# Performance work log

Hardware: AMD Instinct MI355X
Metric: run time of the kernel (lower is better)

Reference implementation:

```python
import jax, jax.numpy as jnp
import numpy as np

B, C, H, W = 2, 128, 64, 64


def setup_inputs() -> dict:
    key = jax.random.key(0)
    ks = jax.random.split(key, 16)
    s = 1.0 / np.sqrt(C)
    d = {
        "x": jax.random.normal(ks[0], (B, C, H, W), jnp.float32),
        "y": jax.random.normal(ks[1], (B, C, H, W), jnp.float32),
    }
    names = ["qr", "qi", "kr", "ki", "vr", "vi"]
    for i, n in enumerate(names):
        d["W" + n] = jax.random.normal(ks[2 + 2 * i], (C, C), jnp.float32) * s
        d["b" + n] = jax.random.normal(ks[3 + 2 * i], (C,), jnp.float32) * s
    return d


def _lin(t, Wt, bt):
    # t: [b, n, c]; torch Linear: t @ W^T + b
    return jnp.einsum("bnc,dc->bnd", t, Wt) + bt


def reference(x, y, Wqr, bqr, Wqi, bqi, Wkr, bkr, Wki, bki, Wvr, bvr, Wvi, bvi):
    b, c, h, w = x.shape
    xf = jnp.fft.fft2(x)  # over last two axes (h, w)
    yf = jnp.fft.fft2(y)
    # b c h w -> b (h w) c
    def flat(t):
        return t.transpose(0, 2, 3, 1).reshape(b, h * w, c)
    xr, xi = flat(xf.real), flat(xf.imag)
    yr, yi = flat(yf.real), flat(yf.imag)

    Qr = _lin(xr, Wqr, bqr) - _lin(xi, Wqi, bqi)
    Qi = _lin(xi, Wqr, bqr) + _lin(xr, Wqi, bqi)
    Kr = _lin(yr, Wkr, bkr) - _lin(yi, Wki, bki)
    Ki = _lin(yi, Wkr, bkr) + _lin(yr, Wki, bki)
    Vr = _lin(yr, Wvr, bvr) - _lin(yi, Wvi, bvi)
    Vi = _lin(yi, Wvr, bvr) + _lin(yr, Wvi, bvi)

    sr = jnp.einsum("bnc,bmc->bnm", Qr, Kr) - jnp.einsum("bnc,bmc->bnm", Qi, Ki)
    si = jnp.einsum("bnc,bmc->bnm", Qr, Ki) + jnp.einsum("bnc,bmc->bnm", Qi, Kr)
    scores = jnp.sqrt(sr * sr + si * si + 1e-8)
    attn = jax.nn.softmax(scores, axis=-1)

    out_r = jnp.einsum("bnm,bmc->bnc", attn, Vr)
    out_i = jnp.einsum("bnm,bmc->bnc", attn, Vi)
    out_c = jax.lax.complex(out_r, out_i)
    # b (h w) c -> b c h w
    out_c = out_c.reshape(b, h, w, c).transpose(0, 3, 1, 2)
    return jnp.fft.ifft2(out_c).real
```

## Files before the change

kernel.cpp:

```cpp
#include <hip/hip_runtime.h>
#include <math.h>


#define PI2 6.283185307179586f

typedef __attribute__((ext_vector_type(8))) short short8;
typedef __attribute__((ext_vector_type(4))) float f32x4;

#define MFMA16(A,B,C) __builtin_amdgcn_mfma_f32_16x16x32_bf16((A),(B),(C),0,0,0)

__device__ inline unsigned short f2bf(float x){
  union{float f; unsigned int u;} a; a.f = x;
  unsigned int r = (a.u + 0x7fffu + ((a.u>>16)&1u)) >> 16;
  return (unsigned short)r;
}
__device__ inline float bf2f(unsigned short h){
  union{unsigned int u; float f;} a; a.u = ((unsigned int)h)<<16; return a.f;
}
__device__ inline short8 neg8(short8 x){
  union{short8 v; unsigned int u[4];} a; a.v = x;
  a.u[0]^=0x80008000u; a.u[1]^=0x80008000u; a.u[2]^=0x80008000u; a.u[3]^=0x80008000u;
  return a.v;
}
__device__ inline void gload_lds16(const void* g, void* lds){
  __builtin_amdgcn_global_load_lds((const __attribute__((address_space(1))) unsigned int*)g,
                                   (__attribute__((address_space(3))) unsigned int*)lds,
                                   16, 0, 0);
}

__global__ __launch_bounds__(256) void dft2_fwd_kernel(
    const float* __restrict__ x, const float* __restrict__ y,
    float* __restrict__ xr, float* __restrict__ xi,
    float* __restrict__ yr, float* __restrict__ yi)
{
  __shared__ float Xs[4096];
  __shared__ float Tr[4096], Ti[4096];
  __shared__ float twc[64], tws[64];
  int blk = blockIdx.x;
  const float* src; float *outr, *outi;
  int plane;
  if (blk < 256) { src = x; outr = xr; outi = xi; plane = blk; }
  else           { src = y; outr = yr; outi = yi; plane = blk - 256; }
  int b = plane >> 7, c = plane & 127;
  int t = threadIdx.x;
  if (t < 64) {
    float ang = -PI2 * (float)t / 64.0f;
    twc[t] = cosf(ang); tws[t] = sinf(ang);
  }
  const float* p = src + ((size_t)plane << 12);
  for (int i = t; i < 4096; i += 256) Xs[i] = p[i];
  __syncthreads();
  for (int j = 0; j < 16; j++) {
    int o = t + 256 * j; int h = o >> 6, wp = o & 63;
    float ar = 0.f, ai = 0.f;
    for (int w = 0; w < 64; w++) {
      int k = (w * wp) & 63;
      float v = Xs[h * 64 + w];
      ar = fmaf(v, twc[k], ar);
      ai = fmaf(v, tws[k], ai);
    }
    Tr[h * 64 + wp] = ar; Ti[h * 64 + wp] = ai;
  }
  __syncthreads();
  size_t ob = ((size_t)b * 4096) * 128 + c;
  for (int j = 0; j < 16; j++) {
    int o = t + 256 * j; int hp = o >> 6, wp = o & 63;
    float ar = 0.f, ai = 0.f;
    for (int h = 0; h < 64; h++) {
      int k = (h * hp) & 63;
      float cr = twc[k], ci = tws[k];
      float tr = Tr[h * 64 + wp], ti = Ti[h * 64 + wp];
      ar += tr * cr - ti * ci;
      ai += tr * ci + ti * cr;
    }
    int n = (hp << 6) + wp;
    outr[ob + (size_t)n * 128] = ar;
    outi[ob + (size_t)n * 128] = ai;
  }
}

__global__ __launch_bounds__(256) void proj_kernel(
    const float* __restrict__ xr, const float* __restrict__ xi,
    const float* __restrict__ yr, const float* __restrict__ yi,
    const float* __restrict__ Wqr, const float* __restrict__ bqr,
    const float* __restrict__ Wqi, const float* __restrict__ bqi,
    const float* __restrict__ Wkr, const float* __restrict__ bkr,
    const float* __restrict__ Wki, const float* __restrict__ bki,
    const float* __restrict__ Wvr, const float* __restrict__ bvr,
    const float* __restrict__ Wvi, const float* __restrict__ bvi,
    unsigned short* __restrict__ FQ, unsigned short* __restrict__ FK,
    unsigned short* __restrict__ FV)
{
  __shared__ float Asr[64 * 33], Asi[64 * 33], Wsr[128 * 33], Wsi[128 * 33];
  int nt = blockIdx.x, lin = blockIdx.y, b = blockIdx.z;
  const float *ar, *ai, *Wr, *Wi, *br_, *bi_;
  unsigned short* F;
  if (lin == 0)      { ar = xr; ai = xi; Wr = Wqr; Wi = Wqi; br_ = bqr; bi_ = bqi; F = FQ; }
  else if (lin == 1) { ar = yr; ai = yi; Wr = Wkr; Wi = Wki; br_ = bkr; bi_ = bki; F = FK; }
  else               { ar = yr; ai = yi; Wr = Wvr; Wi = Wvi; br_ = bvr; bi_ = bvi; F = FV; }
  int t = threadIdx.x; int td = t & 15, tn = t >> 4;
  int n0 = nt * 64;
  size_t abase = (size_t)b * 4096 * 128 + (size_t)n0 * 128;
  const size_t PS = (size_t)2 * 4096 * 128;
  float accr[4][8] = {}, acci[4][8] = {};
  for (int kk = 0; kk < 4; kk++) {
    __syncthreads();
    for (int idx = t; idx < 64 * 32; idx += 256) {
      int r = idx >> 5, ccol = idx & 31;
      Asr[r * 33 + ccol] = ar[abase + (size_t)r * 128 + kk * 32 + ccol];
      Asi[r * 33 + ccol] = ai[abase + (size_t)r * 128 + kk * 32 + ccol];
    }
    for (int idx = t; idx < 128 * 32; idx += 256) {
      int r = idx >> 5, ccol = idx & 31;
      Wsr[r * 33 + ccol] = Wr[(size_t)r * 128 + kk * 32 + ccol];
      Wsi[r * 33 + ccol] = Wi[(size_t)r * 128 + kk * 32 + ccol];
    }
    __syncthreads();
    for (int k = 0; k < 32; k++) {
      float a_r[4], a_i[4], w_r[8], w_i[8];
      #pragma unroll
      for (int i = 0; i < 4; i++) {
        a_r[i] = Asr[(tn * 4 + i) * 33 + k];
        a_i[i] = Asi[(tn * 4 + i) * 33 + k];
      }
      #pragma unroll
      for (int jj = 0; jj < 8; jj++) {
        w_r[jj] = Wsr[(td + 16 * jj) * 33 + k];
        w_i[jj] = Wsi[(td + 16 * jj) * 33 + k];
      }
      #pragma unroll
      for (int i = 0; i < 4; i++)
        #pragma unroll
        for (int jj = 0; jj < 8; jj++) {
          accr[i][jj] += a_r[i] * w_r[jj] - a_i[i] * w_i[jj];
          acci[i][jj] += a_i[i] * w_r[jj] + a_r[i] * w_i[jj];
        }
    }
  }
  for (int jj = 0; jj < 8; jj++) {
    int d = td + 16 * jj;
    float brd = br_[d], bid = bi_[d];
    #pragma unroll
    for (int i = 0; i < 4; i++) {
      int n = n0 + tn * 4 + i;
      float cr = accr[i][jj] + (brd - bid);
      float ci = acci[i][jj] + (brd + bid);
      size_t base = ((size_t)b * 4096 + n) * 128 + d;
      if (lin <= 1) {
        unsigned short rh = f2bf(cr); unsigned short rl = f2bf(cr - bf2f(rh));
        unsigned short ih = f2bf(ci); unsigned short il = f2bf(ci - bf2f(ih));
        F[0 * PS + base] = rh;
        F[1 * PS + base] = rl;
        F[2 * PS + base] = ih;
        F[3 * PS + base] = il;
      } else {
        F[0 * PS + base] = f2bf(cr);
        F[1 * PS + base] = f2bf(ci);
      }
    }
  }
}

__global__ __launch_bounds__(256) void vpack_kernel(
    const unsigned short* __restrict__ F, unsigned short* __restrict__ Vpk)
{
  __shared__ unsigned short Vs[2 * 32 * 128];
  int blk = blockIdx.x;
  int b = blk >> 7, sm = blk & 127;
  int t = threadIdx.x;
  const size_t PS = (size_t)2 * 4096 * 128;
  #pragma unroll
  for (int p = 0; p < 2; p++) {
    #pragma unroll
    for (int k = 0; k < 2; k++) {
      int idx8 = t + 256 * k;
      int nn = idx8 >> 4, d0 = (idx8 & 15) * 8;
      const short8 v = *(const short8*)(F + p * PS + ((size_t)(b * 4096 + sm * 32 + nn)) * 128 + d0);
      *(short8*)(Vs + (p * 32 + nn) * 128 + d0) = v;
    }
  }
  __syncthreads();
  size_t obase = (size_t)blk * 1024;
  #pragma unroll
  for (int k = 0; k < 4; k++) {
    int idx = t + 256 * k;
    int lv = idx & 63, tc = idx >> 6;
    int vh = tc >> 3;
    int d = (tc & 7) * 16 + (lv & 15);
    int nb = (lv >> 4) * 8;
    short8 v;
    #pragma unroll
    for (int j = 0; j < 8; j++)
      v[j] = (short)Vs[(vh * 32 + nb + j) * 128 + d];
    *(short8*)(Vpk + (obase + idx) * 8) = v;
  }
}

__global__ __launch_bounds__(512, 1) void attn_mfma_kernel(
    const unsigned short* __restrict__ FQ, const unsigned short* __restrict__ FK,
    const short* __restrict__ Vpk,
    float* __restrict__ Or_, float* __restrict__ Oi_)
{
  __shared__ __align__(16) short K0lds[32768];
  __shared__ __align__(16) short K1lds[32768];
  __shared__ __align__(16) short Pfrag[2 * 16 * 72];
  __shared__ __align__(16) float rmax[2][16][4];
  __shared__ __align__(16) float escs[2][16];

  const int bi = blockIdx.x;
  const int xg = bi & 7;
  const int b = xg >> 2;
  const int qt = (bi >> 3) * 4 + (xg & 3);
  const int t = threadIdx.x;
  const int w = t >> 6, l = t & 63;
  const int qg = w & 1, ms = w >> 1;
  const int g = l >> 4, c = l & 15;

  const int tq = qt * 2 + qg;
  short8 Qf[4][4];
  #pragma unroll
  for (int a = 0; a < 4; a++)
    #pragma unroll
    for (int s = 0; s < 4; s++)
      Qf[a][s] = *(const short8*)(FQ + (((size_t)((a * 2 + b) * 4096) + tq * 16 + c) * 128 + 32 * s + 8 * g));

  f32x4 O[4], Oe;
  #pragma unroll
  for (int nt = 0; nt < 4; nt++) O[nt] = (f32x4){0.f, 0.f, 0.f, 0.f};
  Oe = (f32x4){0.f, 0.f, 0.f, 0.f};
  float Mq = -3e38f;
  short8 Vreg[2][4];
  const short b1 = (short)0x3F80;
  const short8 ones = {b1, b1, b1, b1, b1, b1, b1, b1};
  const short8* Vp8 = (const short8*)Vpk;

  {
    #pragma unroll
    for (int i2 = 0; i2 < 8; i2++) {
      int ch = w + 8 * i2;
      int a = ch >> 4, rr = ((ch & 15) << 2) + g;
      int u = c ^ (rr & 7);
      gload_lds16(FK + (((size_t)((a * 2 + b) * 4096) + rr) * 128 + u * 8),
                  K0lds + (size_t)ch * 512);
    }
    asm volatile("s_waitcnt vmcnt(0)" ::: "memory");
    __builtin_amdgcn_s_barrier();
    __builtin_amdgcn_sched_barrier(0);
  }

  auto STEP = [&](const short* kb, short* dmadst, int mt) {
    if (mt + 1 < 64) {
      int m0 = (mt + 1) * 64;
      #pragma unroll
      for (int i2 = 0; i2 < 8; i2++) {
        int ch = w + 8 * i2;
        int a = ch >> 4, rr = ((ch & 15) << 2) + g;
        int u = c ^ (rr & 7);
        gload_lds16(FK + (((size_t)((a * 2 + b) * 4096) + m0 + rr) * 128 + u * 8),
                    dmadst + (size_t)ch * 512);
      }
    }
    __builtin_amdgcn_s_setprio(1);
    if (mt > 0) {
      f32x4 ev = *(const f32x4*)&escs[qg][4 * g];
      #pragma unroll
      for (int r = 0; r < 4; r++) {
        #pragma unroll
        for (int nt = 0; nt < 4; nt++) O[nt][r] *= ev[r];
        Oe[r] *= ev[r];
      }
      #pragma unroll
      for (int ks = 0; ks < 2; ks++) {
        short8 Pa = *(const short8*)&Pfrag[(qg * 16 + c) * 72 + 32 * ks + 8 * g];
        #pragma unroll
        for (int nt = 0; nt < 4; nt++)
          O[nt] = MFMA16(Pa, Vreg[ks][nt], O[nt]);
        Oe = MFMA16(Pa, ones, Oe);
      }
    }
    const short8* kb8 = (const short8*)kb;
    f32x4 sr = (f32x4){0, 0, 0, 0}, si = (f32x4){0, 0, 0, 0};
    #pragma unroll
    for (int s = 0; s < 4; s++) {
      int base0 = (ms * 16 + c) * 16 + ((s * 4 + g) ^ (c & 7));
      short8 Arh = kb8[base0];
      short8 Arl = kb8[base0 + 1024];
      short8 Aih = kb8[base0 + 2048];
      short8 Ail = kb8[base0 + 3072];
      short8 nqh = neg8(Qf[2][s]);
      short8 nql = neg8(Qf[3][s]);
      sr = MFMA16(Arh, Qf[0][s], sr);
      si = MFMA16(Arh, Qf[2][s], si);
      sr = MFMA16(Arh, Qf[1][s], sr);
      si = MFMA16(Arh, Qf[3][s], si);
      sr = MFMA16(Arl, Qf[0][s], sr);
      si = MFMA16(Arl, Qf[2][s], si);
      sr = MFMA16(Aih, nqh, sr);
      si = MFMA16(Aih, Qf[0][s], si);
      sr = MFMA16(Aih, nql, sr);
      si = MFMA16(Aih, Qf[1][s], si);
      sr = MFMA16(Ail, nqh, sr);
      si = MFMA16(Ail, Qf[0][s], si);
    }
    __builtin_amdgcn_s_setprio(0);
    f32x4 s0;
    #pragma unroll
    for (int r = 0; r < 4; r++)
      s0[r] = sqrtf(sr[r] * sr[r] + si[r] * si[r] + 1e-8f);
    float mloc = fmaxf(fmaxf(s0[0], s0[1]), fmaxf(s0[2], s0[3]));
    mloc = fmaxf(mloc, __shfl_xor(mloc, 16));
    mloc = fmaxf(mloc, __shfl_xor(mloc, 32));
    if (l < 16) rmax[qg][l][ms] = mloc;
    asm volatile("s_waitcnt lgkmcnt(0)" ::: "memory");
    __builtin_amdgcn_s_barrier();
    __builtin_amdgcn_sched_barrier(0);
    {
      f32x4 rm4 = *(const f32x4*)&rmax[qg][c][0];
      float nmq = fmaxf(fmaxf(rm4[0], rm4[1]), fmaxf(rm4[2], rm4[3]));
      nmq = fmaxf(Mq, nmq);
      float escq = __expf(Mq - nmq);
      Mq = nmq;
      if (ms == 0 && l < 16) escs[qg][l] = escq;
      #pragma unroll
      for (int ks = 0; ks < 2; ks++)
        #pragma unroll
        for (int nt = 0; nt < 4; nt++)
          Vreg[ks][nt] = Vp8[((size_t)((b * 128 + mt * 2 + ks) * 16 + ms * 4 + nt)) * 64 + l];
      f32x4 p;
      #pragma unroll
      for (int r = 0; r < 4; r++) p[r] = __expf(s0[r] - nmq);
      unsigned int w01 = (unsigned int)f2bf(p[0]) | ((unsigned int)f2bf(p[1]) << 16);
      unsigned int w23 = (unsigned int)f2bf(p[2]) | ((unsigned int)f2bf(p[3]) << 16);
      unsigned int* pw = (unsigned int*)&Pfrag[(qg * 16 + c) * 72 + 16 * ms + 4 * g];
      pw[0] = w01; pw[1] = w23;
    }
    asm volatile("s_waitcnt vmcnt(8) lgkmcnt(0)" ::: "memory");
    __builtin_amdgcn_s_barrier();
    __builtin_amdgcn_sched_barrier(0);
  };

  for (int mt = 0; mt < 64; mt += 2) {
    STEP(K0lds, K1lds, mt);
    STEP(K1lds, K0lds, mt + 1);
  }
  {
    f32x4 ev = *(const f32x4*)&escs[qg][4 * g];
    #pragma unroll
    for (int r = 0; r < 4; r++) {
      #pragma unroll
      for (int nt = 0; nt < 4; nt++) O[nt][r] *= ev[r];
      Oe[r] *= ev[r];
    }
    #pragma unroll
    for (int ks = 0; ks < 2; ks++) {
      short8 Pa = *(const short8*)&Pfrag[(qg * 16 + c) * 72 + 32 * ks + 8 * g];
      #pragma unroll
      for (int nt = 0; nt < 4; nt++)
        O[nt] = MFMA16(Pa, Vreg[ks][nt], O[nt]);
      Oe = MFMA16(Pa, ones, Oe);
    }
  }
  const size_t base = (size_t)b * 4096 * 128;
  f32x4 inv;
  #pragma unroll
  for (int r = 0; r < 4; r++) inv[r] = 1.0f / Oe[r];
  #pragma unroll
  for (int nt = 0; nt < 4; nt++) {
    int cc = ms * 64 + nt * 16 + c;
    #pragma unroll
    for (int r = 0; r < 4; r++) {
      int row = qt * 32 + qg * 16 + 4 * g + r;
      float v = O[nt][r] * inv[r];
      if (cc < 128) Or_[base + (size_t)row * 128 + cc] = v;
      else          Oi_[base + (size_t)row * 128 + cc - 128] = v;
    }
  }
}

__global__ __launch_bounds__(256) void idft2_kernel(
    const float* __restrict__ Or_, const float* __restrict__ Oi_,
    float* __restrict__ out)
{
  __shared__ float Ar[4096], Ai[4096], Tr[4096], Ti[4096];
  __shared__ float twc[64], tws[64];
  int plane = blockIdx.x; int b = plane >> 7, c = plane & 127;
  int t = threadIdx.x;
  if (t < 64) {
    float ang = PI2 * (float)t / 64.0f;
    twc[t] = cosf(ang); tws[t] = sinf(ang);
  }
  size_t ibase = (size_t)b * 4096 * 128 + c;
  for (int i = t; i < 4096; i += 256) {
    Ar[i] = Or_[ibase + (size_t)i * 128];
    Ai[i] = Oi_[ibase + (size_t)i * 128];
  }
  __syncthreads();
  for (int j = 0; j < 16; j++) {
    int o = t + 256 * j; int hp = o >> 6, w = o & 63;
    float tr = 0.f, ti = 0.f;
    for (int wp = 0; wp < 64; wp++) {
      int k = (wp * w) & 63;
      float cr = twc[k], ci = tws[k];
      float ar = Ar[hp * 64 + wp], ai = Ai[hp * 64 + wp];
      tr += ar * cr - ai * ci;
      ti += ai * cr + ar * ci;
    }
    Tr[hp * 64 + w] = tr; Ti[hp * 64 + w] = ti;
  }
  __syncthreads();
  size_t obase = ((size_t)plane) << 12;
  for (int j = 0; j < 16; j++) {
    int o = t + 256 * j; int h = o >> 6, w = o & 63;
    float acc = 0.f;
    for (int hp = 0; hp < 64; hp++) {
      int k = (hp * h) & 63;
      acc += Tr[hp * 64 + w] * twc[k] - Ti[hp * 64 + w] * tws[k];
    }
    out[obase + o] = acc * (1.0f / 4096.0f);
  }
}

extern "C" void kernel_launch(void* const* d_in, const int* in_sizes, int n_in,
                              void* d_out, int out_size, void* d_ws, size_t ws_size,
                              hipStream_t stream) {
  const float* x   = (const float*)d_in[0];
  const float* y   = (const float*)d_in[1];
  const float* Wqr = (const float*)d_in[2];  const float* bqr = (const float*)d_in[3];
  const float* Wqi = (const float*)d_in[4];  const float* bqi = (const float*)d_in[5];
  const float* Wkr = (const float*)d_in[6];  const float* bkr = (const float*)d_in[7];
  const float* Wki = (const float*)d_in[8];  const float* bki = (const float*)d_in[9];
  const float* Wvr = (const float*)d_in[10]; const float* bvr = (const float*)d_in[11];
  const float* Wvi = (const float*)d_in[12]; const float* bvi = (const float*)d_in[13];
  char* wsb = (char*)d_ws;
  if (ws_size < ((size_t)40 << 20)) return;
  unsigned short* FQ  = (unsigned short*)(wsb);
  unsigned short* FK  = (unsigned short*)(wsb + ((size_t)8  << 20));
  unsigned short* FV  = (unsigned short*)(wsb + ((size_t)16 << 20));
  float* xr = (float*)(wsb + ((size_t)20 << 20));
  float* xi = (float*)(wsb + ((size_t)24 << 20));
  float* yr = (float*)(wsb + ((size_t)28 << 20));
  float* yi = (float*)(wsb + ((size_t)32 << 20));
  unsigned short* Vpk = (unsigned short*)(wsb + ((size_t)36 << 20));
  float* Or_ = (float*)(wsb + ((size_t)20 << 20));
  float* Oi_ = (float*)(wsb + ((size_t)24 << 20));
  float* out = (float*)d_out;

  hipLaunchKernelGGL(dft2_fwd_kernel, dim3(512), dim3(256), 0, stream,
                     x, y, xr, xi, yr, yi);
  hipLaunchKernelGGL(proj_kernel, dim3(64, 3, 2), dim3(256), 0, stream,
                     xr, xi, yr, yi,
                     Wqr, bqr, Wqi, bqi, Wkr, bkr, Wki, bki, Wvr, bvr, Wvi, bvi,
                     FQ, FK, FV);
  hipLaunchKernelGGL(vpack_kernel, dim3(256), dim3(256), 0, stream, FV, Vpk);
  hipLaunchKernelGGL(attn_mfma_kernel, dim3(256), dim3(512), 0, stream,
                     FQ, FK, (const short*)Vpk, Or_, Oi_);
  hipLaunchKernelGGL(idft2_kernel, dim3(256), dim3(256), 0, stream,
                     Or_, Oi_, out);
}
```

Before: 431.0 us.

## Pre-pack K into MFMA fragment order and run single-buffered attention at two blocks per CU

Adds a kpack kernel that rearranges the K tiles into MFMA fragment order, so the attention kernel can stage them with contiguous 16-byte LDS copies and read them without swizzle arithmetic. The attention kernel moves from 512-thread blocks with two query groups and double-buffered K in LDS to 256-thread blocks with one query group and a single 64KB K buffer. This lets two blocks share a CU across twice as many blocks. The next tile's copy is issued after the max-reduction barrier, and the softmax rescale factor now moves through a shuffle instead of LDS. The cost is an extra launch plus a K-sized copy, and less in-block overlap of loads with compute.

```diff
diff --git a/kernel.cpp b/kernel.cpp
--- a/kernel.cpp
+++ b/kernel.cpp
@@ -161,6 +161,24 @@
   }
 }
 
+__global__ __launch_bounds__(256) void kpack_kernel(
+    const unsigned short* __restrict__ F, unsigned short* __restrict__ Kpk)
+{
+  int blk = blockIdx.x;
+  int b = blk >> 6, mt = blk & 63;
+  int t = threadIdx.x;
+  size_t obase = (size_t)blk * 4096;
+  #pragma unroll
+  for (int k = 0; k < 16; k++) {
+    int idx = t + 256 * k;
+    int l = idx & 63, s = (idx >> 6) & 3, tml = (idx >> 8) & 3, a = idx >> 10;
+    int n = mt * 64 + tml * 16 + (l & 15);
+    int c0 = 32 * s + 8 * (l >> 4);
+    const short8 v = *(const short8*)(F + (((size_t)(a * 2 + b) * 4096 + n) * 128 + c0));
+    *(short8*)(Kpk + (obase + idx) * 8) = v;
+  }
+}
+
 __global__ __launch_bounds__(256) void vpack_kernel(
     const unsigned short* __restrict__ F, unsigned short* __restrict__ Vpk)
 {
@@ -196,97 +214,88 @@
   }
 }
 
-__global__ __launch_bounds__(512, 1) void attn_mfma_kernel(
-    const unsigned short* __restrict__ FQ, const unsigned short* __restrict__ FK,
+__global__ __launch_bounds__(256, 2) void attn_mfma_kernel(
+    const unsigned short* __restrict__ FQ, const short* __restrict__ Kpk,
     const short* __restrict__ Vpk,
     float* __restrict__ Or_, float* __restrict__ Oi_)
 {
-  __shared__ __align__(16) short K0lds[32768];
-  __shared__ __align__(16) short K1lds[32768];
-  __shared__ __align__(16) short Pfrag[2 * 16 * 72];
-  __shared__ __align__(16) float rmax[2][16][4];
-  __shared__ __align__(16) float escs[2][16];
+  __shared__ __align__(16) short Klds[32768];
+  __shared__ __align__(16) short Pfrag[16 * 72];
+  __shared__ __align__(16) float rmax[16][4];
 
   const int bi = blockIdx.x;
   const int xg = bi & 7;
   const int b = xg >> 2;
-  const int qt = (bi >> 3) * 4 + (xg & 3);
+  const int qt2 = (bi >> 3) * 4 + (xg & 3);
   const int t = threadIdx.x;
-  const int w = t >> 6, l = t & 63;
-  const int qg = w & 1, ms = w >> 1;
+  const int ms = t >> 6, l = t & 63;
   const int g = l >> 4, c = l & 15;
 
-  const int tq = qt * 2 + qg;
+  const size_t PS = (size_t)2 * 4096 * 128;
   short8 Qf[4][4];
   #pragma unroll
   for (int a = 0; a < 4; a++)
     #pragma unroll
     for (int s = 0; s < 4; s++)
-      Qf[a][s] = *(const short8*)(FQ + (((size_t)((a * 2 + b) * 4096) + tq * 16 + c) * 128 + 32 * s + 8 * g));
+      Qf[a][s] = *(const short8*)(FQ + (size_t)a * PS +
+                 ((size_t)(b * 4096) + qt2 * 16 + c) * 128 + 32 * s + 8 * g);
 
   f32x4 O[4], Oe;
   #pragma unroll
   for (int nt = 0; nt < 4; nt++) O[nt] = (f32x4){0.f, 0.f, 0.f, 0.f};
   Oe = (f32x4){0.f, 0.f, 0.f, 0.f};
-  float Mq = -3e38f;
+  float Mq = -3e38f, escPrev = 1.0f;
   short8 Vreg[2][4];
   const short b1 = (short)0x3F80;
   const short8 ones = {b1, b1, b1, b1, b1, b1, b1, b1};
   const short8* Vp8 = (const short8*)Vpk;
 
-  {
-    #pragma unroll
-    for (int i2 = 0; i2 < 8; i2++) {
-      int ch = w + 8 * i2;
-      int a = ch >> 4, rr = ((ch & 15) << 2) + g;
-      int u = c ^ (rr & 7);
-      gload_lds16(FK + (((size_t)((a * 2 + b) * 4096) + rr) * 128 + u * 8),
-                  K0lds + (size_t)ch * 512);
-    }
-    asm volatile("s_waitcnt vmcnt(0)" ::: "memory");
-    __builtin_amdgcn_s_barrier();
-    __builtin_amdgcn_sched_barrier(0);
-  }
-
-  auto STEP = [&](const short* kb, short* dmadst, int mt) {
-    if (mt + 1 < 64) {
-      int m0 = (mt + 1) * 64;
-      #pragma unroll
-      for (int i2 = 0; i2 < 8; i2++) {
-        int ch = w + 8 * i2;
-        int a = ch >> 4, rr = ((ch & 15) << 2) + g;
-        int u = c ^ (rr & 7);
-        gload_lds16(FK + (((size_t)((a * 2 + b) * 4096) + m0 + rr) * 128 + u * 8),
-                    dmadst + (size_t)ch * 512);
-      }
-    }
-    __builtin_amdgcn_s_setprio(1);
+  auto STAGE = [&](int tile) {
+    const char* gsrc = (const char*)Kpk + ((size_t)(b * 64 + tile) << 16);
+    #pragma unroll
+    for (int i2 = 0; i2 < 16; i2++) {
+      int ch = ms * 16 + i2;
+      gload_lds16(gsrc + ch * 1024 + l * 16, (char*)Klds + ch * 1024);
+    }
+  };
+
+  STAGE(0);
+  asm volatile("s_waitcnt vmcnt(0)" ::: "memory");
+  __builtin_amdgcn_s_barrier();
+  __builtin_amdgcn_sched_barrier(0);
+
+  f32x4 s0;
+  for (int mt = 0; mt < 64; mt++) {
     if (mt > 0) {
-      f32x4 ev = *(const f32x4*)&escs[qg][4 * g];
+      f32x4 esc4;
+      #pragma unroll
+      for (int r = 0; r < 4; r++) esc4[r] = __shfl(escPrev, 4 * g + r);
       #pragma unroll
       for (int r = 0; r < 4; r++) {
         #pragma unroll
-        for (int nt = 0; nt < 4; nt++) O[nt][r] *= ev[r];
-        Oe[r] *= ev[r];
+        for (int nt = 0; nt < 4; nt++) O[nt][r] *= esc4[r];
+        Oe[r] *= esc4[r];
       }
+      __builtin_amdgcn_s_setprio(1);
       #pragma unroll
       for (int ks = 0; ks < 2; ks++) {
-        short8 Pa = *(const short8*)&Pfrag[(qg * 16 + c) * 72 + 32 * ks + 8 * g];
+        short8 Pa = *(const short8*)&Pfrag[c * 72 + 32 * ks + 8 * g];
         #pragma unroll
         for (int nt = 0; nt < 4; nt++)
           O[nt] = MFMA16(Pa, Vreg[ks][nt], O[nt]);
         Oe = MFMA16(Pa, ones, Oe);
       }
-    }
-    const short8* kb8 = (const short8*)kb;
+      __builtin_amdgcn_s_setprio(0);
+    }
+    const short8* kb8 = (const short8*)Klds;
     f32x4 sr = (f32x4){0, 0, 0, 0}, si = (f32x4){0, 0, 0, 0};
+    __builtin_amdgcn_s_setprio(1);
     #pragma unroll
     for (int s = 0; s < 4; s++) {
-      int base0 = (ms * 16 + c) * 16 + ((s * 4 + g) ^ (c & 7));
-      short8 Arh = kb8[base0];
-      short8 Arl = kb8[base0 + 1024];
-      short8 Aih = kb8[base0 + 2048];
-      short8 Ail = kb8[base0 + 3072];
+      short8 Arh = kb8[((0 * 4 + ms) * 4 + s) * 64 + l];
+      short8 Arl = kb8[((1 * 4 + ms) * 4 + s) * 64 + l];
+      short8 Aih = kb8[((2 * 4 + ms) * 4 + s) * 64 + l];
+      short8 Ail = kb8[((3 * 4 + ms) * 4 + s) * 64 + l];
       short8 nqh = neg8(Qf[2][s]);
       short8 nql = neg8(Qf[3][s]);
       sr = MFMA16(Arh, Qf[0][s], sr);
@@ -303,57 +312,53 @@
       si = MFMA16(Ail, Qf[0][s], si);
     }
     __builtin_amdgcn_s_setprio(0);
-    f32x4 s0;
     #pragma unroll
     for (int r = 0; r < 4; r++)
       s0[r] = sqrtf(sr[r] * sr[r] + si[r] * si[r] + 1e-8f);
     float mloc = fmaxf(fmaxf(s0[0], s0[1]), fmaxf(s0[2], s0[3]));
     mloc = fmaxf(mloc, __shfl_xor(mloc, 16));
     mloc = fmaxf(mloc, __shfl_xor(mloc, 32));
-    if (l < 16) rmax[qg][l][ms] = mloc;
+    if (l < 16) rmax[l][ms] = mloc;
     asm volatile("s_waitcnt lgkmcnt(0)" ::: "memory");
     __builtin_amdgcn_s_barrier();
     __builtin_amdgcn_sched_barrier(0);
+    if (mt + 1 < 64) STAGE(mt + 1);
     {
-      f32x4 rm4 = *(const f32x4*)&rmax[qg][c][0];
-      float nmq = fmaxf(fmaxf(rm4[0], rm4[1]), fmaxf(rm4[2], rm4[3]));
-      nmq = fmaxf(Mq, nmq);
-      float escq = __expf(Mq - nmq);
-      Mq = nmq;
-      if (ms == 0 && l < 16) escs[qg][l] = escq;
+      f32x4 rm4 = *(const f32x4*)&rmax[c][0];
+      float Mnew = fmaxf(fmaxf(rm4[0], rm4[1]), fmaxf(rm4[2], rm4[3]));
+      Mnew = fmaxf(Mq, Mnew);
+      escPrev = __expf(Mq - Mnew);
+      Mq = Mnew;
+      f32x4 p;
+      #pragma unroll
+      for (int r = 0; r < 4; r++) p[r] = __expf(s0[r] - Mnew);
+      unsigned int* pw = (unsigned int*)&Pfrag[c * 72 + 16 * ms + 4 * g];
+      pw[0] = (unsigned int)f2bf(p[0]) | ((unsigned int)f2bf(p[1]) << 16);
+      pw[1] = (unsigned int)f2bf(p[2]) | ((unsigned int)f2bf(p[3]) << 16);
       #pragma unroll
       for (int ks = 0; ks < 2; ks++)
         #pragma unroll
         for (int nt = 0; nt < 4; nt++)
           Vreg[ks][nt] = Vp8[((size_t)((b * 128 + mt * 2 + ks) * 16 + ms * 4 + nt)) * 64 + l];
-      f32x4 p;
-      #pragma unroll
-      for (int r = 0; r < 4; r++) p[r] = __expf(s0[r] - nmq);
-      unsigned int w01 = (unsigned int)f2bf(p[0]) | ((unsigned int)f2bf(p[1]) << 16);
-      unsigned int w23 = (unsigned int)f2bf(p[2]) | ((unsigned int)f2bf(p[3]) << 16);
-      unsigned int* pw = (unsigned int*)&Pfrag[(qg * 16 + c) * 72 + 16 * ms + 4 * g];
-      pw[0] = w01; pw[1] = w23;
-    }
+    }
+    __builtin_amdgcn_sched_barrier(0);
     asm volatile("s_waitcnt vmcnt(8) lgkmcnt(0)" ::: "memory");
     __builtin_amdgcn_s_barrier();
     __builtin_amdgcn_sched_barrier(0);
-  };
-
-  for (int mt = 0; mt < 64; mt += 2) {
-    STEP(K0lds, K1lds, mt);
-    STEP(K1lds, K0lds, mt + 1);
   }
   {
-    f32x4 ev = *(const f32x4*)&escs[qg][4 * g];
+    f32x4 esc4;
+    #pragma unroll
+    for (int r = 0; r < 4; r++) esc4[r] = __shfl(escPrev, 4 * g + r);
     #pragma unroll
     for (int r = 0; r < 4; r++) {
       #pragma unroll
-      for (int nt = 0; nt < 4; nt++) O[nt][r] *= ev[r];
-      Oe[r] *= ev[r];
+      for (int nt = 0; nt < 4; nt++) O[nt][r] *= esc4[r];
+      Oe[r] *= esc4[r];
     }
     #pragma unroll
     for (int ks = 0; ks < 2; ks++) {
-      short8 Pa = *(const short8*)&Pfrag[(qg * 16 + c) * 72 + 32 * ks + 8 * g];
+      short8 Pa = *(const short8*)&Pfrag[c * 72 + 32 * ks + 8 * g];
       #pragma unroll
       for (int nt = 0; nt < 4; nt++)
         O[nt] = MFMA16(Pa, Vreg[ks][nt], O[nt]);
@@ -369,7 +374,7 @@
     int cc = ms * 64 + nt * 16 + c;
     #pragma unroll
     for (int r = 0; r < 4; r++) {
-      int row = qt * 32 + qg * 16 + 4 * g + r;
+      int row = qt2 * 16 + 4 * g + r;
       float v = O[nt][r] * inv[r];
       if (cc < 128) Or_[base + (size_t)row * 128 + cc] = v;
       else          Oi_[base + (size_t)row * 128 + cc - 128] = v;
@@ -440,6 +445,7 @@
   float* xi = (float*)(wsb + ((size_t)24 << 20));
   float* yr = (float*)(wsb + ((size_t)28 << 20));
   float* yi = (float*)(wsb + ((size_t)32 << 20));
+  unsigned short* Kpk = (unsigned short*)(wsb + ((size_t)28 << 20));
   unsigned short* Vpk = (unsigned short*)(wsb + ((size_t)36 << 20));
   float* Or_ = (float*)(wsb + ((size_t)20 << 20));
   float* Oi_ = (float*)(wsb + ((size_t)24 << 20));
@@ -451,9 +457,10 @@
                      xr, xi, yr, yi,
                      Wqr, bqr, Wqi, bqi, Wkr, bkr, Wki, bki, Wvr, bvr, Wvi, bvi,
                      FQ, FK, FV);
+  hipLaunchKernelGGL(kpack_kernel, dim3(128), dim3(256), 0, stream, FK, Kpk);
   hipLaunchKernelGGL(vpack_kernel, dim3(256), dim3(256), 0, stream, FV, Vpk);
-  hipLaunchKernelGGL(attn_mfma_kernel, dim3(256), dim3(512), 0, stream,
-                     FQ, FK, (const short*)Vpk, Or_, Oi_);
+  hipLaunchKernelGGL(attn_mfma_kernel, dim3(512), dim3(256), 0, stream,
+                     FQ, (const short*)Kpk, (const short*)Vpk, Or_, Oi_);
   hipLaunchKernelGGL(idft2_kernel, dim3(256), dim3(256), 0, stream,
                      Or_, Oi_, out);
 }
```

Result: faster. 406.5 us (-5.7%).
